# Optimization experiments

Measured on AMD Instinct MI355X. Metric: run time of the kernel, lower is better.

## Reference

```python
import jax, jax.numpy as jnp
import numpy as np
import math

N = 100000
E = 1600000
IN_DIM = 64
OUT_DIM = 64
EPS = 1e-5


def setup_inputs() -> dict:
    key = jax.random.key(0)
    ks = jax.random.split(key, 12)
    s = 1.0 / math.sqrt(IN_DIM)
    inp = {
        "geo_x": jax.random.normal(ks[0], (N, IN_DIM), dtype=jnp.float32),
        "euc_x": jax.random.normal(ks[1], (N, IN_DIM), dtype=jnp.float32),
        "Wq": jax.random.uniform(ks[2], (OUT_DIM, IN_DIM), minval=-s, maxval=s, dtype=jnp.float32),
        "bq": jnp.zeros((OUT_DIM,), jnp.float32),
        "Wk": jax.random.uniform(ks[3], (OUT_DIM, IN_DIM), minval=-s, maxval=s, dtype=jnp.float32),
        "bk": jnp.zeros((OUT_DIM,), jnp.float32),
        "Wv": jax.random.uniform(ks[4], (OUT_DIM, IN_DIM), minval=-s, maxval=s, dtype=jnp.float32),
        "bv": jnp.zeros((OUT_DIM,), jnp.float32),
        "Wskip": jax.random.uniform(ks[5], (OUT_DIM, IN_DIM), minval=-s, maxval=s, dtype=jnp.float32),
        "bskip": jnp.zeros((OUT_DIM,), jnp.float32),
        "ln_w": jnp.ones((OUT_DIM,), jnp.float32),
        "ln_b": jnp.zeros((OUT_DIM,), jnp.float32),
        "edge_index": jax.random.randint(ks[6], (2, E), 0, N, dtype=jnp.int64),
    }
    return inp


def reference(geo_x, euc_x, Wq, bq, Wk, bk, Wv, bv, Wskip, bskip, ln_w, ln_b, edge_index):
    n = euc_x.shape[0]
    src, dst = edge_index[0], edge_index[1]

    # TransformerConv, heads=1: q from target (euc), k/v from source (geo)
    q = euc_x @ Wq.T + bq                      # [N, C]
    k = geo_x @ Wk.T + bk                      # [N, C]
    v = geo_x @ Wv.T + bv                      # [N, C]
    C = q.shape[-1]

    # per-edge attention logits
    alpha = jnp.sum(q[dst] * k[src], axis=-1) / math.sqrt(C)   # [E]

    # segment softmax over incoming edges of each destination node
    amax = jax.ops.segment_max(alpha, dst, num_segments=n)
    amax = jnp.where(jnp.isfinite(amax), amax, 0.0)
    ex = jnp.exp(alpha - amax[dst])
    denom = jax.ops.segment_sum(ex, dst, num_segments=n)
    w = ex / (denom[dst] + 1e-16)                              # [E]

    # scatter-aggregate weighted values + root (skip) transform
    agg = jax.ops.segment_sum(w[:, None] * v[src], dst, num_segments=n)  # [N, C]
    out = agg + euc_x @ Wskip.T + bskip

    # PyG LayerNorm, mode='graph', batch=None: normalize over all nodes+channels
    mean = out.mean()
    xc = out - mean
    std = jnp.sqrt(jnp.mean(xc * xc))
    out = xc / (std + EPS) * ln_w + ln_b

    return jax.nn.relu(out)
```

## Files before the change

### kernel.cpp

```cpp
#include <hip/hip_runtime.h>
#include <hip/hip_fp16.h>


using short8 = __attribute__((ext_vector_type(8))) short;
using f32x4  = __attribute__((ext_vector_type(4))) float;
using h2     = __attribute__((ext_vector_type(2))) _Float16;
using u32x4  = __attribute__((ext_vector_type(4))) unsigned;
using u32x2  = __attribute__((ext_vector_type(2))) unsigned;
using f32x4v = __attribute__((ext_vector_type(4))) float;

#define QSCALE 31.75f
#define VDESC  0.031496062992f
#define SCI    1.7889250e-4f

#define CAP   4608
#define NCBMAX 400

__device__ inline int ntload(const int* p) {
    return __builtin_nontemporal_load(p);
}
__device__ inline unsigned ntload(const unsigned* p) {
    return __builtin_nontemporal_load(p);
}
__device__ inline uint2 ntload(const uint2* p) {
    u32x2 v = __builtin_nontemporal_load((const u32x2*)p);
    return make_uint2(v.x, v.y);
}
__device__ inline uint4 ntload(const uint4* p) {
    u32x4 v = __builtin_nontemporal_load((const u32x4*)p);
    return make_uint4(v.x, v.y, v.z, v.w);
}
__device__ inline float4 ntload(const float4* p) {
    f32x4v v = __builtin_nontemporal_load((const f32x4v*)p);
    return make_float4(v.x, v.y, v.z, v.w);
}
__device__ inline void ntstore(unsigned* p, unsigned v) {
    __builtin_nontemporal_store(v, p);
}
__device__ inline void ntstore(uint4* p, uint4 v) {
    u32x4 t; t.x = v.x; t.y = v.y; t.z = v.z; t.w = v.w;
    __builtin_nontemporal_store(t, (u32x4*)p);
}
__device__ inline void ntstore(float4* p, float4 v) {
    f32x4v t; t.x = v.x; t.y = v.y; t.z = v.z; t.w = v.w;
    __builtin_nontemporal_store(t, (f32x4v*)p);
}

__device__ inline unsigned short f2bf(float f) {
    unsigned u = __float_as_uint(f);
    unsigned r = u + 0x7FFFu + ((u >> 16) & 1u);
    return (unsigned short)(r >> 16);
}
__device__ inline unsigned short f2h(float f) {
    union { _Float16 h; unsigned short u; } c;
    c.h = (_Float16)f;
    return c.u;
}
__device__ inline h2 u2h2(unsigned u) {
    union { unsigned u; h2 h; } c; c.u = u; return c.h;
}
__device__ inline signed char f2i8(float f) {
    float v = f * QSCALE;
    v = fminf(fmaxf(v, -127.f), 127.f);
    return (signed char)__float2int_rn(v);
}

__device__ inline float fexp2(float x) {
#if __has_builtin(__builtin_amdgcn_exp2f)
    return __builtin_amdgcn_exp2f(x);
#else
    return __expf(x * 0.6931471805599453f);
#endif
}

__device__ inline int dot8i(uint2 q, uint2 k) {
#if __has_builtin(__builtin_amdgcn_sdot4)
    int t = __builtin_amdgcn_sdot4((int)q.x, (int)k.x, 0, false);
    return  __builtin_amdgcn_sdot4((int)q.y, (int)k.y, t, false);
#else
    int t = 0;
    #pragma unroll
    for (int i = 0; i < 4; ++i) {
        int qa = (int)(q.x << (24 - 8 * i)) >> 24;
        int ka = (int)(k.x << (24 - 8 * i)) >> 24;
        int qb = (int)(q.y << (24 - 8 * i)) >> 24;
        int kb = (int)(k.y << (24 - 8 * i)) >> 24;
        t += qa * ka + qb * kb;
    }
    return t;
#endif
}

__global__ __launch_bounds__(256) void k0_wconv(
    const float* __restrict__ Wq, const float* __restrict__ Wk,
    const float* __restrict__ Wv, const float* __restrict__ Wsk,
    unsigned short* __restrict__ wbf, int* __restrict__ zbase, int zcount)
{
    if (blockIdx.x == 16) {
        for (int i = threadIdx.x; i < zcount; i += 256) zbase[i] = 0;
        return;
    }
    int mat = blockIdx.x >> 2;
    int i4  = (blockIdx.x & 3) * 256 + threadIdx.x;
    const float* W = (mat == 0) ? Wq : (mat == 1) ? Wk : (mat == 2) ? Wv : Wsk;
    float4 w = *(const float4*)(W + (long)i4 * 4);
    ushort4 o;
    o.x = f2bf(w.x); o.y = f2bf(w.y); o.z = f2bf(w.z); o.w = f2bf(w.w);
    *(ushort4*)(wbf + (long)mat * 4096 + (long)i4 * 4) = o;
}

__global__ __launch_bounds__(256, 3) void k1_proj(
    const float* __restrict__ geo, const float* __restrict__ euc,
    const unsigned short* __restrict__ wbf,
    const float* __restrict__ bq, const float* __restrict__ bk,
    const float* __restrict__ bv, const float* __restrict__ bsk,
    signed char* __restrict__ q8b, signed char* __restrict__ kv8,
    unsigned short* __restrict__ skb, int N)
{
    __shared__ __align__(16) char smem[2 * 64 * 208];
    const int tid  = threadIdx.x;
    const int lane = tid & 63;
    const int w    = tid >> 6;
    const int qq   = lane >> 4;
    const int m    = lane & 15;
    const long base = (long)blockIdx.x * 128;

    char* t0 = smem;
    char* t1 = smem + 64 * 208;

    const long nodeA0 = base + w * 16 + m;
    const long nodeA1 = base + 64 + w * 16 + m;

    auto loadA = [&](const float* __restrict__ x, long node, short8 a[2]) {
        const float* px = x + node * 64;
        const bool v = (node < N);
        #pragma unroll
        for (int kh = 0; kh < 2; ++kh) {
            float4 f0 = v ? ntload((const float4*)(px + kh * 32 + qq * 8))
                          : make_float4(0.f, 0.f, 0.f, 0.f);
            float4 f1 = v ? ntload((const float4*)(px + kh * 32 + qq * 8 + 4))
                          : make_float4(0.f, 0.f, 0.f, 0.f);
            short8 r;
            r[0] = (short)f2bf(f0.x); r[1] = (short)f2bf(f0.y);
            r[2] = (short)f2bf(f0.z); r[3] = (short)f2bf(f0.w);
            r[4] = (short)f2bf(f1.x); r[5] = (short)f2bf(f1.y);
            r[6] = (short)f2bf(f1.z); r[7] = (short)f2bf(f1.w);
            a[kh] = r;
        }
    };
    auto loadB = [&](int mat, short8 b[2][4]) {
        #pragma unroll
        for (int kh = 0; kh < 2; ++kh)
            #pragma unroll
            for (int nt = 0; nt < 4; ++nt)
                b[kh][nt] = *(const short8*)(wbf + (long)mat * 4096 +
                                             (nt * 16 + m) * 64 + kh * 32 + qq * 8);
    };
    auto mmul = [&](const short8 a[2], const short8 b[2][4], f32x4 acc[4]) {
        #pragma unroll
        for (int nt = 0; nt < 4; ++nt) acc[nt] = (f32x4)(0.f);
        #pragma unroll
        for (int kh = 0; kh < 2; ++kh)
            #pragma unroll
            for (int nt = 0; nt < 4; ++nt)
                acc[nt] = __builtin_amdgcn_mfma_f32_16x16x32_bf16(a[kh], b[kh][nt], acc[nt], 0, 0, 0);
    };

    auto emit_i8 = [&](const f32x4 acc[4], const float* __restrict__ bias, char* tile) {
        #pragma unroll
        for (int nt = 0; nt < 4; ++nt) {
            int c = nt * 16 + m;
            float bs = bias[c];
            #pragma unroll
            for (int r = 0; r < 4; ++r) {
                int nl = w * 16 + qq * 4 + r;
                *(signed char*)(tile + nl * 208 + c) = f2i8(acc[nt][r] + bs);
            }
        }
    };
    auto emit_h = [&](const f32x4 acc[4], const float* __restrict__ bias, char* tile) {
        #pragma unroll
        for (int nt = 0; nt < 4; ++nt) {
            int c = nt * 16 + m;
            float bs = bias[c];
            #pragma unroll
            for (int r = 0; r < 4; ++r) {
                int nl = w * 16 + qq * 4 + r;
                *(unsigned short*)(tile + nl * 208 + 64 + c * 2) = f2h(acc[nt][r] + bs);
            }
        }
    };
    auto emit_kv = [&](const f32x4 acc[4], const float* __restrict__ bias,
                       char* tile, int vpart) {
        #pragma unroll
        for (int nt = 0; nt < 4; ++nt) {
            int c = nt * 16 + m;
            float bs = bias[c];
            int boff = (c >> 3) * 16 + vpart * 8 + (c & 7);
            #pragma unroll
            for (int r = 0; r < 4; ++r) {
                int nl = w * 16 + qq * 4 + r;
                *(signed char*)(tile + nl * 208 + boff) = f2i8(acc[nt][r] + bs);
            }
        }
    };

    short8 a0[2], a1[2];
    short8 B0[2][4], B1[2][4];
    f32x4 acc[4];

    loadA(euc, nodeA0, a0);
    loadA(euc, nodeA1, a1);
    loadB(0, B0);
    loadB(3, B1);
    mmul(a0, B0, acc); emit_i8(acc, bq, t0);
    mmul(a1, B0, acc); emit_i8(acc, bq, t1);
    mmul(a0, B1, acc); emit_h(acc, bsk, t0);
    mmul(a1, B1, acc); emit_h(acc, bsk, t1);
    __syncthreads();
    #pragma unroll
    for (int t = 0; t < 2; ++t) {
        const char* te = t ? t1 : t0;
        const long tb = base + t * 64;
        {
            int n = tid >> 2, j = tid & 3;
            long nd = tb + n;
            if (nd < N)
                *(int4*)(q8b + nd * 64 + j * 16) = *(const int4*)(te + n * 208 + j * 16);
        }
        #pragma unroll
        for (int it = 0; it < 2; ++it) {
            int idx = it * 256 + tid;
            int n = idx >> 3, j = idx & 7;
            long nd = tb + n;
            if (nd < N)
                *(int4*)((char*)skb + nd * 128 + j * 16) =
                    *(const int4*)(te + n * 208 + 64 + j * 16);
        }
    }
    __syncthreads();

    loadA(geo, nodeA0, a0);
    loadA(geo, nodeA1, a1);
    loadB(1, B0);
    loadB(2, B1);
    mmul(a0, B0, acc); emit_kv(acc, bk, t0, 0);
    mmul(a1, B0, acc); emit_kv(acc, bk, t1, 0);
    mmul(a0, B1, acc); emit_kv(acc, bv, t0, 1);
    mmul(a1, B1, acc); emit_kv(acc, bv, t1, 1);
    __syncthreads();
    #pragma unroll
    for (int t = 0; t < 2; ++t) {
        const char* tg = t ? t1 : t0;
        const long tb = base + t * 64;
        #pragma unroll
        for (int it = 0; it < 2; ++it) {
            int idx = it * 256 + tid;
            int n = idx >> 3, j = idx & 7;
            long nd = tb + n;
            if (nd < N)
                *(int4*)(kv8 + nd * 128 + j * 16) = *(const int4*)(tg + n * 208 + j * 16);
        }
    }
}

__global__ __launch_bounds__(512) void k2a_part(
    const int* __restrict__ ei, int E, int N,
    int* __restrict__ ccur, unsigned* __restrict__ tmp)
{
    __shared__ unsigned ebuf[4096];
    __shared__ unsigned short cbuf[4096];
    __shared__ int h[NCBMAX], offA[NCBMAX], lc[NCBMAX], creg[NCBMAX];
    __shared__ int sc[512];

    const int tid = threadIdx.x;
    const int NCB = (N + 255) >> 8;
    const long e0 = (long)blockIdx.x * 4096;
    const int tileN = (int)(((long)E - e0 < 4096) ? ((long)E - e0) : 4096);

    for (int i = tid; i < NCB; i += 512) { h[i] = 0; lc[i] = 0; }
    __syncthreads();

    const int* srcp = ei;
    const int* dstp = ei + E;
    unsigned wj[8];
    int cbj[8];
    #pragma unroll
    for (int j = 0; j < 8; ++j) {
        int i = j * 512 + tid;
        wj[j] = 0u; cbj[j] = -1;
        if (i < tileN) {
            int d = ntload(&dstp[e0 + i]), s = ntload(&srcp[e0 + i]);
            cbj[j] = d >> 8;
            wj[j]  = ((unsigned)(d & 255) << 17) | (unsigned)s;
            atomicAdd(&h[cbj[j]], 1);
        }
    }
    __syncthreads();

    sc[tid] = (tid < NCB) ? h[tid] : 0;
    __syncthreads();
    int own = sc[tid];
    for (int off = 1; off < 512; off <<= 1) {
        int v = (tid >= off) ? sc[tid - off] : 0;
        __syncthreads();
        sc[tid] += v;
        __syncthreads();
    }
    if (tid < NCB) offA[tid] = sc[tid] - own;
    if (tid < NCB && h[tid] > 0)
        creg[tid] = atomicAdd(&ccur[tid], h[tid]);
    __syncthreads();

    #pragma unroll
    for (int j = 0; j < 8; ++j) {
        if (cbj[j] >= 0) {
            int pos = offA[cbj[j]] + atomicAdd(&lc[cbj[j]], 1);
            ebuf[pos] = wj[j];
            cbuf[pos] = (unsigned short)cbj[j];
        }
    }
    __syncthreads();

    #pragma unroll
    for (int j = 0; j < 8; ++j) {
        int i = j * 512 + tid;
        if (i < tileN) {
            int cb = cbuf[i];
            int r  = creg[cb] + (i - offA[cb]);
            if (r < CAP) ntstore(&tmp[(long)cb * CAP + r], ebuf[i]);
        }
    }
}

__global__ __launch_bounds__(512, 8) void k3_attn(
    const signed char* __restrict__ q8b, const signed char* __restrict__ kv8,
    const unsigned short* __restrict__ skb,
    const int* __restrict__ ccnt, const unsigned* __restrict__ tmp,
    unsigned short* __restrict__ preb,
    float* __restrict__ partS, float* __restrict__ partSS, int N)
{
    __shared__ unsigned bkt[128 * 65];
    __shared__ int dcnt[128];
    __shared__ unsigned char perm[128];
    __shared__ float redS[8], redSS[8];
    const int tid  = threadIdx.x;
    const int lane = tid & 63;
    const int w    = tid >> 6;
    const int g0   = tid >> 3;
    const int gl   = tid & 7;
    const int bin  = blockIdx.x;
    const int cb   = bin >> 1;
    const unsigned sub = (unsigned)(bin & 1);
    const long nodeBase = (long)bin * 128;

    if (tid < 128) dcnt[tid] = 0;
    __syncthreads();

    int len = ccnt[cb];
    if (len > CAP) len = CAP;
    const unsigned* reg = tmp + (long)cb * CAP;
    for (int e = tid; e < len; e += 512) {
        unsigned wv = ntload(&reg[e]);
        if (((wv >> 24) & 1u) == sub) {
            int d = (wv >> 17) & 127;
            int slot = atomicAdd(&dcnt[d], 1);
            if (slot < 64) bkt[d * 65 + slot] = wv & 0x1FFFFu;
        }
    }
    __syncthreads();

    if (tid < 128) {
        int d = dcnt[tid]; if (d > 64) d = 64;
        int r = 0;
        for (int j = 0; j < 128; ++j) {
            int dj = dcnt[j]; if (dj > 64) dj = 64;
            r += (dj > d) || ((dj == d) && (j < tid));
        }
        perm[r] = (unsigned char)tid;
    }
    __syncthreads();

    float sacc = 0.f, ssacc = 0.f;

    for (int half = 0; half < 2; ++half) {
        const int row  = perm[half ? (127 - g0) : g0];
        const long node = nodeBase + row;

        uint2 qu = make_uint2(0, 0);
        if (node < N) qu = ntload((const uint2*)(q8b + node * 64 + gl * 8));

        int deg = dcnt[row];
        if (deg > 64) deg = 64;

        float den = 0.f;
        float a0=0.f,a1=0.f,a2=0.f,a3=0.f,a4=0.f,a5=0.f,a6=0.f,a7=0.f;

        auto vacc = [&](unsigned vx, unsigned vy, float ex) {
            a0 = fmaf((float)((int)(vx << 24) >> 24), ex, a0);
            a1 = fmaf((float)((int)(vx << 16) >> 24), ex, a1);
            a2 = fmaf((float)((int)(vx <<  8) >> 24), ex, a2);
            a3 = fmaf((float)((int)(vx      ) >> 24), ex, a3);
            a4 = fmaf((float)((int)(vy << 24) >> 24), ex, a4);
            a5 = fmaf((float)((int)(vy << 16) >> 24), ex, a5);
            a6 = fmaf((float)((int)(vy <<  8) >> 24), ex, a6);
            a7 = fmaf((float)((int)(vy      ) >> 24), ex, a7);
        };

        if (deg > 0) {
            const int rb  = row * 65;
            const int dm1 = deg - 1;
            unsigned sA = bkt[rb];
            uint4 rA = *(const uint4*)(kv8 + (long)sA * 128 + gl * 16);

            for (int s = 0; s < deg; s += 2) {
                int i1 = (s + 1 < deg) ? s + 1 : dm1;
                unsigned sB = bkt[rb + i1];
                uint4 rB = *(const uint4*)(kv8 + (long)sB * 128 + gl * 16);

                int t0 = dot8i(qu, make_uint2(rA.x, rA.y));
                t0 += __shfl_xor(t0, 1);
                t0 += __shfl_xor(t0, 2);
                t0 += __shfl_xor(t0, 4);
                float ex0 = fexp2((float)t0 * SCI);
                den += ex0;
                vacc(rA.z, rA.w, ex0);

                int i2 = (s + 2 < deg) ? s + 2 : dm1;
                unsigned sC = bkt[rb + i2];
                rA = *(const uint4*)(kv8 + (long)sC * 128 + gl * 16);

                int t1 = dot8i(qu, make_uint2(rB.x, rB.y));
                t1 += __shfl_xor(t1, 1);
                t1 += __shfl_xor(t1, 2);
                t1 += __shfl_xor(t1, 4);
                float ex1 = (s + 1 < deg) ? fexp2((float)t1 * SCI) : 0.f;
                den += ex1;
                vacc(rB.z, rB.w, ex1);
            }
        }

        if (node < N) {
            float inv = VDESC / (den + 1e-16f);
            uint4 sk = ntload((const uint4*)((const char*)skb + node * 128 + gl * 16));
            h2 s0 = u2h2(sk.x), s1 = u2h2(sk.y), s2 = u2h2(sk.z), s3 = u2h2(sk.w);
            float o0 = a0 * inv + (float)s0.x, o1 = a1 * inv + (float)s0.y;
            float o2 = a2 * inv + (float)s1.x, o3 = a3 * inv + (float)s1.y;
            float o4 = a4 * inv + (float)s2.x, o5 = a5 * inv + (float)s2.y;
            float o6 = a6 * inv + (float)s3.x, o7 = a7 * inv + (float)s3.y;
            uint4 ov;
            ov.x = (unsigned)f2h(o0) | ((unsigned)f2h(o1) << 16);
            ov.y = (unsigned)f2h(o2) | ((unsigned)f2h(o3) << 16);
            ov.z = (unsigned)f2h(o4) | ((unsigned)f2h(o5) << 16);
            ov.w = (unsigned)f2h(o6) | ((unsigned)f2h(o7) << 16);
            ntstore((uint4*)((char*)preb + node * 128 + gl * 16), ov);
            sacc  += (o0 + o1 + o2 + o3) + (o4 + o5 + o6 + o7);
            ssacc += o0*o0 + o1*o1 + o2*o2 + o3*o3 + o4*o4 + o5*o5 + o6*o6 + o7*o7;
        }
    }

    #pragma unroll
    for (int m = 1; m <= 32; m <<= 1) {
        sacc  += __shfl_xor(sacc, m);
        ssacc += __shfl_xor(ssacc, m);
    }
    if (lane == 0) { redS[w] = sacc; redSS[w] = ssacc; }
    __syncthreads();
    if (tid == 0) {
        float s = 0.f, ss = 0.f;
        #pragma unroll
        for (int i = 0; i < 8; ++i) { s += redS[i]; ss += redSS[i]; }
        partS[bin]  = s;
        partSS[bin] = ss;
    }
}

__global__ __launch_bounds__(256) void k35_stats(
    const float* __restrict__ partS, const float* __restrict__ partSS,
    int nparts, float* __restrict__ stats, float M)
{
    __shared__ float rs[256], rss[256];
    float s = 0.f, ss = 0.f;
    for (int i = threadIdx.x; i < nparts; i += 256) { s += partS[i]; ss += partSS[i]; }
    rs[threadIdx.x] = s; rss[threadIdx.x] = ss;
    __syncthreads();
    for (int st = 128; st > 0; st >>= 1) {
        if (threadIdx.x < st) {
            rs[threadIdx.x]  += rs[threadIdx.x + st];
            rss[threadIdx.x] += rss[threadIdx.x + st];
        }
        __syncthreads();
    }
    if (threadIdx.x == 0) {
        float mean = rs[0] / M;
        float var  = rss[0] / M - mean * mean;
        if (var < 0.f) var = 0.f;
        stats[0] = mean;
        stats[1] = 1.f / (sqrtf(var) + 1e-5f);
    }
}

__global__ __launch_bounds__(256) void k4_ln(
    const unsigned short* __restrict__ preb, float* __restrict__ out,
    const float* __restrict__ lnw, const float* __restrict__ lnb,
    const float* __restrict__ stats, int M8)
{
    int i = blockIdx.x * 256 + threadIdx.x;
    if (i >= M8) return;
    float mean = stats[0], scale = stats[1];
    uint4 pv = ntload((const uint4*)((const char*)preb + (size_t)i * 16));
    int c8 = (i & 7) * 8;
    float4 w0 = *(const float4*)(lnw + c8);
    float4 w1 = *(const float4*)(lnw + c8 + 4);
    float4 b0 = *(const float4*)(lnb + c8);
    float4 b1 = *(const float4*)(lnb + c8 + 4);
    h2 p0 = u2h2(pv.x), p1 = u2h2(pv.y), p2 = u2h2(pv.z), p3 = u2h2(pv.w);
    float4 r0, r1;
    r0.x = fmaxf(((float)p0.x - mean) * scale * w0.x + b0.x, 0.f);
    r0.y = fmaxf(((float)p0.y - mean) * scale * w0.y + b0.y, 0.f);
    r0.z = fmaxf(((float)p1.x - mean) * scale * w0.z + b0.z, 0.f);
    r0.w = fmaxf(((float)p1.y - mean) * scale * w0.w + b0.w, 0.f);
    r1.x = fmaxf(((float)p2.x - mean) * scale * w1.x + b1.x, 0.f);
    r1.y = fmaxf(((float)p2.y - mean) * scale * w1.y + b1.y, 0.f);
    r1.z = fmaxf(((float)p3.x - mean) * scale * w1.z + b1.z, 0.f);
    r1.w = fmaxf(((float)p3.y - mean) * scale * w1.w + b1.w, 0.f);
    ntstore((float4*)(out + (size_t)i * 8), r0);
    ntstore((float4*)(out + (size_t)i * 8 + 4), r1);
}

extern "C" void kernel_launch(void* const* d_in, const int* in_sizes, int n_in,
                              void* d_out, int out_size, void* d_ws, size_t ws_size,
                              hipStream_t stream)
{
    const float* geo = (const float*)d_in[0];
    const float* euc = (const float*)d_in[1];
    const float* Wq  = (const float*)d_in[2];
    const float* bq  = (const float*)d_in[3];
    const float* Wk  = (const float*)d_in[4];
    const float* bk  = (const float*)d_in[5];
    const float* Wv  = (const float*)d_in[6];
    const float* bv  = (const float*)d_in[7];
    const float* Wsk = (const float*)d_in[8];
    const float* bsk = (const float*)d_in[9];
    const float* lnw = (const float*)d_in[10];
    const float* lnb = (const float*)d_in[11];
    const int*   ei  = (const int*)d_in[12];

    const int N = in_sizes[0] / 64;
    const int E = in_sizes[12] / 2;
    const int KB = (N + 127) / 128;
    const int NCB = (N + 255) >> 8;
    float* out = (float*)d_out;

    char* p = (char*)d_ws;
    signed char*    q8b   = (signed char*)p;    p += (size_t)N * 64;
    signed char*    kv8   = (signed char*)p;    p += (size_t)N * 128;
    unsigned short* skb   = (unsigned short*)p; p += (size_t)N * 64 * 2;
    unsigned short* preb  = (unsigned short*)p; p += (size_t)N * 64 * 2;
    unsigned*       tmp   = (unsigned*)p;       p += (size_t)NCB * CAP * 4;
    unsigned short* wbf   = (unsigned short*)p; p += (size_t)4 * 4096 * 2;
    int* ccur = (int*)p;  p += (size_t)(NCB + 8) * 4;
    float* partS  = (float*)p; p += (size_t)KB * 4;
    float* partSS = (float*)p; p += (size_t)KB * 4;
    float* stats  = (float*)p;

    const int PB2 = (N + 127) / 128;

    k0_wconv<<<17, 256, 0, stream>>>(Wq, Wk, Wv, Wsk, wbf, ccur, NCB + 8);
    k1_proj<<<PB2, 256, 0, stream>>>(geo, euc, wbf, bq, bk, bv, bsk,
                                     q8b, kv8, skb, N);
    const int GA = (E + 4095) / 4096;
    k2a_part<<<GA, 512, 0, stream>>>(ei, E, N, ccur, tmp);
    k3_attn<<<KB, 512, 0, stream>>>(q8b, kv8, skb, ccur, tmp, preb,
                                    partS, partSS, N);
    k35_stats<<<1, 256, 0, stream>>>(partS, partSS, KB, stats, (float)N * 64.0f);
    const int M8 = N * 8;
    k4_ln<<<(M8 + 255) / 256, 256, 0, stream>>>(preb, out, lnw, lnb, stats, M8);
}
```

Measured before the change: 210.7 us.

## Split attention bins into 64-node blocks and cut projection register use

The attention kernel now handles 64 destination nodes per 256-thread block instead of 128 per 512-thread block. It picks its quarter of each 256-node column bucket with two bits of the packed edge word, so each block rescans the full bucket list. This halves LDS per block and doubles the grid, aiming for better occupancy and load balance, at the cost of reading each bucket four times instead of twice. The projection kernel reuses one B-fragment register set instead of two and raises the occupancy hint from 3 to 4, trading some load/compute overlap for fewer registers.

```diff
diff --git a/kernel.cpp b/kernel.cpp
--- a/kernel.cpp
+++ b/kernel.cpp
@@ -109,7 +109,7 @@
     *(ushort4*)(wbf + (long)mat * 4096 + (long)i4 * 4) = o;
 }
 
-__global__ __launch_bounds__(256, 3) void k1_proj(
+__global__ __launch_bounds__(256, 4) void k1_proj(
     const float* __restrict__ geo, const float* __restrict__ euc,
     const unsigned short* __restrict__ wbf,
     const float* __restrict__ bq, const float* __restrict__ bk,
@@ -206,17 +206,17 @@
     };
 
     short8 a0[2], a1[2];
-    short8 B0[2][4], B1[2][4];
+    short8 B[2][4];
     f32x4 acc[4];
 
     loadA(euc, nodeA0, a0);
     loadA(euc, nodeA1, a1);
-    loadB(0, B0);
-    loadB(3, B1);
-    mmul(a0, B0, acc); emit_i8(acc, bq, t0);
-    mmul(a1, B0, acc); emit_i8(acc, bq, t1);
-    mmul(a0, B1, acc); emit_h(acc, bsk, t0);
-    mmul(a1, B1, acc); emit_h(acc, bsk, t1);
+    loadB(0, B);
+    mmul(a0, B, acc); emit_i8(acc, bq, t0);
+    mmul(a1, B, acc); emit_i8(acc, bq, t1);
+    loadB(3, B);
+    mmul(a0, B, acc); emit_h(acc, bsk, t0);
+    mmul(a1, B, acc); emit_h(acc, bsk, t1);
     __syncthreads();
     #pragma unroll
     for (int t = 0; t < 2; ++t) {
@@ -242,12 +242,12 @@
 
     loadA(geo, nodeA0, a0);
     loadA(geo, nodeA1, a1);
-    loadB(1, B0);
-    loadB(2, B1);
-    mmul(a0, B0, acc); emit_kv(acc, bk, t0, 0);
-    mmul(a1, B0, acc); emit_kv(acc, bk, t1, 0);
-    mmul(a0, B1, acc); emit_kv(acc, bv, t0, 1);
-    mmul(a1, B1, acc); emit_kv(acc, bv, t1, 1);
+    loadB(1, B);
+    mmul(a0, B, acc); emit_kv(acc, bk, t0, 0);
+    mmul(a1, B, acc); emit_kv(acc, bk, t1, 0);
+    loadB(2, B);
+    mmul(a0, B, acc); emit_kv(acc, bv, t0, 1);
+    mmul(a1, B, acc); emit_kv(acc, bv, t1, 1);
     __syncthreads();
     #pragma unroll
     for (int t = 0; t < 2; ++t) {
@@ -333,47 +333,47 @@
     }
 }
 
-__global__ __launch_bounds__(512, 8) void k3_attn(
+__global__ __launch_bounds__(256, 8) void k3_attn(
     const signed char* __restrict__ q8b, const signed char* __restrict__ kv8,
     const unsigned short* __restrict__ skb,
     const int* __restrict__ ccnt, const unsigned* __restrict__ tmp,
     unsigned short* __restrict__ preb,
     float* __restrict__ partS, float* __restrict__ partSS, int N)
 {
-    __shared__ unsigned bkt[128 * 65];
-    __shared__ int dcnt[128];
-    __shared__ unsigned char perm[128];
-    __shared__ float redS[8], redSS[8];
+    __shared__ unsigned bkt[64 * 65];
+    __shared__ int dcnt[64];
+    __shared__ unsigned char perm[64];
+    __shared__ float redS[4], redSS[4];
     const int tid  = threadIdx.x;
     const int lane = tid & 63;
     const int w    = tid >> 6;
     const int g0   = tid >> 3;
     const int gl   = tid & 7;
     const int bin  = blockIdx.x;
-    const int cb   = bin >> 1;
-    const unsigned sub = (unsigned)(bin & 1);
-    const long nodeBase = (long)bin * 128;
-
-    if (tid < 128) dcnt[tid] = 0;
+    const int cb   = bin >> 2;
+    const unsigned sub = (unsigned)(bin & 3);
+    const long nodeBase = (long)bin * 64;
+
+    if (tid < 64) dcnt[tid] = 0;
     __syncthreads();
 
     int len = ccnt[cb];
     if (len > CAP) len = CAP;
     const unsigned* reg = tmp + (long)cb * CAP;
-    for (int e = tid; e < len; e += 512) {
+    for (int e = tid; e < len; e += 256) {
         unsigned wv = ntload(&reg[e]);
-        if (((wv >> 24) & 1u) == sub) {
-            int d = (wv >> 17) & 127;
+        if (((wv >> 23) & 3u) == sub) {
+            int d = (wv >> 17) & 63;
             int slot = atomicAdd(&dcnt[d], 1);
             if (slot < 64) bkt[d * 65 + slot] = wv & 0x1FFFFu;
         }
     }
     __syncthreads();
 
-    if (tid < 128) {
+    if (tid < 64) {
         int d = dcnt[tid]; if (d > 64) d = 64;
         int r = 0;
-        for (int j = 0; j < 128; ++j) {
+        for (int j = 0; j < 64; ++j) {
             int dj = dcnt[j]; if (dj > 64) dj = 64;
             r += (dj > d) || ((dj == d) && (j < tid));
         }
@@ -384,7 +384,7 @@
     float sacc = 0.f, ssacc = 0.f;
 
     for (int half = 0; half < 2; ++half) {
-        const int row  = perm[half ? (127 - g0) : g0];
+        const int row  = perm[half ? (63 - g0) : g0];
         const long node = nodeBase + row;
 
         uint2 qu = make_uint2(0, 0);
@@ -469,7 +469,7 @@
     if (tid == 0) {
         float s = 0.f, ss = 0.f;
         #pragma unroll
-        for (int i = 0; i < 8; ++i) { s += redS[i]; ss += redSS[i]; }
+        for (int i = 0; i < 4; ++i) { s += redS[i]; ss += redSS[i]; }
         partS[bin]  = s;
         partSS[bin] = ss;
     }
@@ -548,7 +548,7 @@
 
     const int N = in_sizes[0] / 64;
     const int E = in_sizes[12] / 2;
-    const int KB = (N + 127) / 128;
+    const int K = (N + 63) / 64;
     const int NCB = (N + 255) >> 8;
     float* out = (float*)d_out;
 
@@ -560,8 +560,8 @@
     unsigned*       tmp   = (unsigned*)p;       p += (size_t)NCB * CAP * 4;
     unsigned short* wbf   = (unsigned short*)p; p += (size_t)4 * 4096 * 2;
     int* ccur = (int*)p;  p += (size_t)(NCB + 8) * 4;
-    float* partS  = (float*)p; p += (size_t)KB * 4;
-    float* partSS = (float*)p; p += (size_t)KB * 4;
+    float* partS  = (float*)p; p += (size_t)K * 4;
+    float* partSS = (float*)p; p += (size_t)K * 4;
     float* stats  = (float*)p;
 
     const int PB2 = (N + 127) / 128;
@@ -571,9 +571,9 @@
                                      q8b, kv8, skb, N);
     const int GA = (E + 4095) / 4096;
     k2a_part<<<GA, 512, 0, stream>>>(ei, E, N, ccur, tmp);
-    k3_attn<<<KB, 512, 0, stream>>>(q8b, kv8, skb, ccur, tmp, preb,
-                                    partS, partSS, N);
-    k35_stats<<<1, 256, 0, stream>>>(partS, partSS, KB, stats, (float)N * 64.0f);
+    k3_attn<<<K, 256, 0, stream>>>(q8b, kv8, skb, ccur, tmp, preb,
+                                   partS, partSS, N);
+    k35_stats<<<1, 256, 0, stream>>>(partS, partSS, K, stats, (float)N * 64.0f);
     const int M8 = N * 8;
     k4_ln<<<(M8 + 255) / 256, 256, 0, stream>>>(preb, out, lnw, lnb, stats, M8);
 }
```

Result: no change. 210.8 us, median of 2 (+0.0%).
